# Kernel tuning notes

Hardware: AMD Instinct MI355X
Metric: run time of the kernel (lower is better)

Reference implementation:

```python
import jax, jax.numpy as jnp
import numpy as np

N_LAYERS, H, D, DH = 4, 16, 1024, 64
V_FR, V_EN = 32000, 32000
L_FR, L_EN, B = 513, 512, 2


def _pos_enc(x):
    # x: [L, B, D]; pe[i,j] = sin(i/10000^(j/D)) if j even else cos(i/10000^((j-1)/D))
    L, _, D_ = x.shape
    pos = jnp.arange(L, dtype=jnp.float32)[:, None]
    j = jnp.arange(D_)
    ang = pos / jnp.power(10000.0, (j - (j % 2)).astype(jnp.float32) / D_)
    pe = jnp.where(j % 2 == 0, jnp.sin(ang), jnp.cos(ang))
    return x + pe[:, None, :]


def _ln(x, g, b):
    mu = jnp.mean(x, -1, keepdims=True)
    var = jnp.mean((x - mu) ** 2, -1, keepdims=True)
    return (x - mu) * jax.lax.rsqrt(var + 1e-5) * g + b


def _mha(q_in, k_in, v_in, w, bias, causal):
    # w: [3, H, D, dh], bias: [3, H, dh]
    dh = w.shape[-1]
    Q = jnp.einsum('bld,hde->bhle', q_in, w[0]) + bias[0][None, :, None, :]
    K = jnp.einsum('bmd,hde->bhme', k_in, w[1]) + bias[1][None, :, None, :]
    V = jnp.einsum('bmd,hde->bhme', v_in, w[2]) + bias[2][None, :, None, :]
    s = jnp.einsum('bhle,bhme->bhlm', Q, K) / jnp.sqrt(jnp.float32(dh))
    if causal:
        m = jnp.tril(jnp.ones((s.shape[-2], s.shape[-1]), bool))
        s = jnp.where(m, s, -jnp.inf)
    a = jax.nn.softmax(s, axis=-1)
    o = jnp.einsum('bhlm,bhme->bhle', a, V)
    b_, h_, l_, dh_ = o.shape
    return o.transpose(0, 2, 1, 3).reshape(b_, l_, h_ * dh_)


def setup_inputs() -> dict:
    key = jax.random.key(0)
    ks = jax.random.split(key, 24)
    s = 0.02
    rn = lambda k, shp: jax.random.normal(k, shp, jnp.float32) * s
    return {
        'fr': jax.random.randint(ks[0], (L_FR, B), 0, V_FR),
        'en': jax.random.randint(ks[1], (L_EN, B), 0, V_EN),
        'emb_fr': rn(ks[2], (V_FR, D)),
        'emb_en': rn(ks[3], (V_EN, D)),
        'enc_qkv_w': rn(ks[4], (N_LAYERS, 3, H, D, DH)),
        'enc_qkv_b': rn(ks[5], (N_LAYERS, 3, H, DH)),
        'enc_fc1_w': rn(ks[6], (N_LAYERS, D, D)),
        'enc_fc1_b': rn(ks[7], (N_LAYERS, D)),
        'enc_fc2_w': rn(ks[8], (N_LAYERS, D, D)),
        'enc_fc2_b': rn(ks[9], (N_LAYERS, D)),
        'enc_ln_g': jnp.ones((N_LAYERS, 2, D)) + rn(ks[10], (N_LAYERS, 2, D)),
        'enc_ln_b': rn(ks[11], (N_LAYERS, 2, D)),
        'dec_self_qkv_w': rn(ks[12], (N_LAYERS, 3, H, D, DH)),
        'dec_self_qkv_b': rn(ks[13], (N_LAYERS, 3, H, DH)),
        'dec_cross_qkv_w': rn(ks[14], (N_LAYERS, 3, H, D, DH)),
        'dec_cross_qkv_b': rn(ks[15], (N_LAYERS, 3, H, DH)),
        'dec_fc1_w': rn(ks[16], (N_LAYERS, D, D)),
        'dec_fc1_b': rn(ks[17], (N_LAYERS, D)),
        'dec_fc2_w': rn(ks[18], (N_LAYERS, D, D)),
        'dec_fc2_b': rn(ks[19], (N_LAYERS, D)),
        'dec_ln_g': jnp.ones((N_LAYERS, 3, D)) + rn(ks[20], (N_LAYERS, 3, D)),
        'dec_ln_b': rn(ks[21], (N_LAYERS, 3, D)),
        'out_w': rn(ks[22], (D, V_EN)),
        'out_b': rn(ks[23], (V_EN,)),
    }


def reference(fr, en, emb_fr, emb_en, enc_qkv_w, enc_qkv_b, enc_fc1_w, enc_fc1_b,
              enc_fc2_w, enc_fc2_b, enc_ln_g, enc_ln_b, dec_self_qkv_w,
              dec_self_qkv_b, dec_cross_qkv_w, dec_cross_qkv_b, dec_fc1_w,
              dec_fc1_b, dec_fc2_w, dec_fc2_b, dec_ln_g, dec_ln_b, out_w, out_b):
    # Encoder (dropout p=0 -> identity in eval math)
    x = _pos_enc(emb_fr[fr[1:]]).transpose(1, 0, 2)  # [B, L_src, D]
    for n in range(N_LAYERS):
        a = _mha(x, x, x, enc_qkv_w[n], enc_qkv_b[n], causal=False)
        x = _ln(x + a, enc_ln_g[n, 0], enc_ln_b[n, 0])
        h = jnp.maximum(x @ enc_fc1_w[n] + enc_fc1_b[n], 0.0) @ enc_fc2_w[n] + enc_fc2_b[n]
        x = _ln(x + h, enc_ln_g[n, 1], enc_ln_b[n, 1])
    enc_out = x
    # Decoder
    y = _pos_enc(emb_en[en]).transpose(1, 0, 2)  # [B, L_tgt, D]
    for n in range(N_LAYERS):
        a = _mha(y, y, y, dec_self_qkv_w[n], dec_self_qkv_b[n], causal=True)
        y = _ln(y + a, dec_ln_g[n, 0], dec_ln_b[n, 0])
        c = _mha(y, enc_out, enc_out, dec_cross_qkv_w[n], dec_cross_qkv_b[n], causal=False)
        y = _ln(y + c, dec_ln_g[n, 1], dec_ln_b[n, 1])
        h = jnp.maximum(y @ dec_fc1_w[n] + dec_fc1_b[n], 0.0) @ dec_fc2_w[n] + dec_fc2_b[n]
        y = _ln(y + h, dec_ln_g[n, 2], dec_ln_b[n, 2])
    return y @ out_w + out_b  # [B, L_tgt, V_EN]
```

## Files before the change

kernel.cpp:

```cpp
#include <hip/hip_runtime.h>
#include <stdint.h>
#include <stddef.h>

typedef unsigned short u16;
typedef __attribute__((ext_vector_type(8))) short bf16x8;
typedef __attribute__((ext_vector_type(4))) float f32x4;

#define DEV __device__ __forceinline__

DEV float b2f(u16 u) { union { float f; uint32_t i; } v; v.i = ((uint32_t)u) << 16; return v.f; }
DEV u16 f2b(float f) {
  uint32_t x = __float_as_uint(f);
  x += 0x7fffu + ((x >> 16) & 1u);
  return (u16)(x >> 16);
}
DEV bf16x8 ld8f(const float* f) {
  float4 a = *(const float4*)f;
  float4 b = *(const float4*)(f + 4);
  bf16x8 r;
  ((u16*)&r)[0] = f2b(a.x); ((u16*)&r)[1] = f2b(a.y);
  ((u16*)&r)[2] = f2b(a.z); ((u16*)&r)[3] = f2b(a.w);
  ((u16*)&r)[4] = f2b(b.x); ((u16*)&r)[5] = f2b(b.y);
  ((u16*)&r)[6] = f2b(b.z); ((u16*)&r)[7] = f2b(b.w);
  return r;
}
DEV void gload16(const u16* g, u16* l) {
  __builtin_amdgcn_global_load_lds((const __attribute__((address_space(1))) void*)g,
                                   (__attribute__((address_space(3))) void*)l, 16, 0, 0);
}
DEV f32x4 mfma16(bf16x8 a, bf16x8 b, f32x4 c) {
  return __builtin_amdgcn_mfma_f32_16x16x32_bf16(a, b, c, 0, 0, 0);
}

__global__ __launch_bounds__(256) void transpose_w(const float* __restrict__ src,
                                                   u16* __restrict__ dst, int K, int N) {
  __shared__ u16 t[32][33];
  int tx = threadIdx.x, ty = threadIdx.y;
  int k0 = blockIdx.x * 32, n0 = blockIdx.y * 32;
  size_t base = (size_t)blockIdx.z * K * N;
#pragma unroll
  for (int i = 0; i < 4; i++) {
    int k = ty + 8 * i;
    t[k][tx] = f2b(src[base + (size_t)(k0 + k) * N + n0 + tx]);
  }
  __syncthreads();
#pragma unroll
  for (int i = 0; i < 4; i++) {
    int n = ty + 8 * i;
    dst[base + (size_t)(n0 + n) * K + k0 + tx] = t[tx][n];
  }
}

__global__ __launch_bounds__(256) void transpose_qkvT(const float* __restrict__ s0,
                                                      const float* __restrict__ s1,
                                                      const float* __restrict__ s2,
                                                      u16* __restrict__ dst) {
  int z = blockIdx.z;
  const float* src = (z < 192) ? s0 : (z < 384) ? s1 : s2;
  int zi = (z < 192) ? z : (z < 384) ? z - 192 : z - 384;
  size_t sbase = (size_t)zi * 65536;
  size_t dbase = (size_t)z * 65536;
  __shared__ u16 t[32][33];
  int tx = threadIdx.x, ty = threadIdx.y;
  int k0 = blockIdx.x * 32, n0 = blockIdx.y * 32;
#pragma unroll
  for (int i = 0; i < 4; i++) {
    int k = ty + 8 * i;
    t[k][tx] = f2b(src[sbase + (size_t)(k0 + k) * 64 + n0 + tx]);
  }
  __syncthreads();
#pragma unroll
  for (int i = 0; i < 4; i++) {
    int n = ty + 8 * i;
    dst[dbase + (size_t)(n0 + n) * 1024 + k0 + tx] = t[tx][n];
  }
}

__global__ __launch_bounds__(256) void transpose_fcT(const float* __restrict__ s0,
                                                     const float* __restrict__ s1,
                                                     const float* __restrict__ s2,
                                                     const float* __restrict__ s3,
                                                     u16* __restrict__ dst) {
  int z = blockIdx.z;
  const float* src = (z < 4) ? s0 : (z < 8) ? s1 : (z < 12) ? s2 : s3;
  size_t sbase = (size_t)(z & 3) * 1048576;
  size_t dbase = (size_t)z * 1048576;
  __shared__ u16 t[32][33];
  int tx = threadIdx.x, ty = threadIdx.y;
  int k0 = blockIdx.x * 32, n0 = blockIdx.y * 32;
#pragma unroll
  for (int i = 0; i < 4; i++) {
    int k = ty + 8 * i;
    t[k][tx] = f2b(src[sbase + (size_t)(k0 + k) * 1024 + n0 + tx]);
  }
  __syncthreads();
#pragma unroll
  for (int i = 0; i < 4; i++) {
    int n = ty + 8 * i;
    dst[dbase + (size_t)(n0 + n) * 1024 + k0 + tx] = t[tx][n];
  }
}

__global__ __launch_bounds__(256) void embed_k(const int* __restrict__ tok, const float* __restrict__ emb,
                                               float* __restrict__ o32, u16* __restrict__ ob, int shift) {
  int row = blockIdx.x;
  int b = row >> 9, l = row & 511;
  int tk = tok[(size_t)(l + shift) * 2 + b];
  const float* e = emb + (size_t)tk * 1024;
  const float c0 = -9.210340371976184f / 1024.f;
#pragma unroll
  for (int i = 0; i < 4; i++) {
    int d = threadIdx.x + i * 256;
    int j2 = d & ~1;
    float ang = (float)l * expf(c0 * (float)j2);
    float pe = (d & 1) ? cosf(ang) : sinf(ang);
    float rv = e[d] + pe;
    o32[(size_t)row * 1024 + d] = rv;
    ob[(size_t)row * 1024 + d] = f2b(rv);
  }
}

__global__ __launch_bounds__(256) void ln_k(const float* d,
                                            const float* __restrict__ g, const float* __restrict__ bb,
                                            float* o32, u16* __restrict__ ob) {
  int row = blockIdx.x;
  int tid = threadIdx.x;
  const float4 dv = ((const float4*)(d + (size_t)row * 1024))[tid];
  float v[4] = {dv.x, dv.y, dv.z, dv.w};
  float s = 0.f, s2 = 0.f;
#pragma unroll
  for (int i = 0; i < 4; i++) { s += v[i]; s2 += v[i] * v[i]; }
#pragma unroll
  for (int off = 1; off < 64; off <<= 1) {
    s += __shfl_xor(s, off);
    s2 += __shfl_xor(s2, off);
  }
  __shared__ float red[8];
  int wid = tid >> 6;
  if ((tid & 63) == 0) { red[wid * 2] = s; red[wid * 2 + 1] = s2; }
  __syncthreads();
  s = red[0] + red[2] + red[4] + red[6];
  s2 = red[1] + red[3] + red[5] + red[7];
  float mu = s * (1.f / 1024.f);
  float var = s2 * (1.f / 1024.f) - mu * mu;
  float inv = rsqrtf(var + 1e-5f);
  const float4 gv = ((const float4*)g)[tid];
  const float4 bv = ((const float4*)bb)[tid];
  float4 ov;
  ov.x = (v[0] - mu) * inv * gv.x + bv.x;
  ov.y = (v[1] - mu) * inv * gv.y + bv.y;
  ov.z = (v[2] - mu) * inv * gv.z + bv.z;
  ov.w = (v[3] - mu) * inv * gv.w + bv.w;
  ((float4*)(o32 + (size_t)row * 1024))[tid] = ov;
  uint2 p;
  p.x = (uint32_t)f2b(ov.x) | ((uint32_t)f2b(ov.y) << 16);
  p.y = (uint32_t)f2b(ov.z) | ((uint32_t)f2b(ov.w) << 16);
  ((uint2*)(ob + (size_t)row * 1024))[tid] = p;
}

template <bool RELU>
__global__ __launch_bounds__(256) void gemm_fc(const u16* __restrict__ A, const u16* __restrict__ BT,
                                               const float* __restrict__ bias,
                                               const float* __restrict__ resid, void* __restrict__ out,
                                               int N, int K) {
  __shared__ __align__(16) u16 lA[2][2][64 * 32];
  __shared__ __align__(16) u16 lB[2][2][64 * 32];
  int bx = blockIdx.x, by = blockIdx.y;
  int tid = threadIdx.x, lane = tid & 63, wid = tid >> 6;
  int l15 = lane & 15, lg = lane >> 4;
  int bm = by * 64, bn = bx * 64;
  int wr = (wid >> 1) * 32, wc = (wid & 1) * 32;
  f32x4 acc[2][2] = {};
  int r_s = tid >> 2, c_s = tid & 3;
  auto stage = [&](int pp, int kt) {
#pragma unroll
    for (int s = 0; s < 2; s++) {
      gload16(A + (size_t)(bm + r_s) * K + kt + s * 32 + c_s * 8, &lA[pp][s][(size_t)(wid * 64) * 8]);
      gload16(BT + (size_t)(bn + r_s) * K + kt + s * 32 + c_s * 8, &lB[pp][s][(size_t)(wid * 64) * 8]);
    }
  };
  int nt = K >> 6;
  stage(0, 0);
  int pp = 0;
  for (int t = 0; t < nt; t++) {
    if (t + 1 < nt) {
      stage(pp ^ 1, (t + 1) * 64);
      asm volatile("s_waitcnt vmcnt(4)" ::: "memory");
    } else {
      asm volatile("s_waitcnt vmcnt(0)" ::: "memory");
    }
    __builtin_amdgcn_s_barrier();
#pragma unroll
    for (int s = 0; s < 2; s++) {
      bf16x8 af[2], bf_[2];
#pragma unroll
      for (int m = 0; m < 2; m++) af[m] = *(const bf16x8*)&lA[pp][s][(wr + m * 16 + l15) * 32 + lg * 8];
#pragma unroll
      for (int n = 0; n < 2; n++) bf_[n] = *(const bf16x8*)&lB[pp][s][(wc + n * 16 + l15) * 32 + lg * 8];
#pragma unroll
      for (int m = 0; m < 2; m++)
#pragma unroll
        for (int n = 0; n < 2; n++) acc[m][n] = mfma16(af[m], bf_[n], acc[m][n]);
    }
    __builtin_amdgcn_s_barrier();
    pp ^= 1;
  }
#pragma unroll
  for (int n = 0; n < 2; n++) {
    int col = bn + wc + n * 16 + l15;
    float bv = bias[col];
#pragma unroll
    for (int m = 0; m < 2; m++) {
#pragma unroll
      for (int r = 0; r < 4; r++) {
        int row = bm + wr + m * 16 + lg * 4 + r;
        float v = acc[m][n][r] + bv;
        if (RELU) ((u16*)out)[(size_t)row * N + col] = f2b(fmaxf(v, 0.f));
        else ((float*)out)[(size_t)row * N + col] = v + resid[(size_t)row * N + col];
      }
    }
  }
}

__global__ __launch_bounds__(256) void gemm_qkv3(const u16* __restrict__ Aq, const u16* __restrict__ Akv,
                                                 const u16* __restrict__ WT, const float* __restrict__ bias,
                                                 u16* __restrict__ Qo, u16* __restrict__ Ko,
                                                 u16* __restrict__ Vto) {
  __shared__ __align__(16) u16 lA[2][2][64 * 32];
  __shared__ __align__(16) u16 lB[2][2][64 * 32];
  int bx = blockIdx.x, by = blockIdx.y;
  int t_ = bx >> 4;
  const u16* A = (t_ == 0) ? Aq : Akv;
  int tid = threadIdx.x, lane = tid & 63, wid = tid >> 6;
  int l15 = lane & 15, lg = lane >> 4;
  int bm = by * 64, bn = bx * 64;
  int wr = (wid >> 1) * 32, wc = (wid & 1) * 32;
  f32x4 acc[2][2] = {};
  int r_s = tid >> 2, c_s = tid & 3;
  auto stage = [&](int pp, int kt) {
#pragma unroll
    for (int s = 0; s < 2; s++) {
      gload16(A + (size_t)(bm + r_s) * 1024 + kt + s * 32 + c_s * 8, &lA[pp][s][(size_t)(wid * 64) * 8]);
      gload16(WT + (size_t)(bn + r_s) * 1024 + kt + s * 32 + c_s * 8, &lB[pp][s][(size_t)(wid * 64) * 8]);
    }
  };
  stage(0, 0);
  int pp = 0;
  for (int t = 0; t < 16; t++) {
    if (t + 1 < 16) {
      stage(pp ^ 1, (t + 1) * 64);
      asm volatile("s_waitcnt vmcnt(4)" ::: "memory");
    } else {
      asm volatile("s_waitcnt vmcnt(0)" ::: "memory");
    }
    __builtin_amdgcn_s_barrier();
#pragma unroll
    for (int s = 0; s < 2; s++) {
      bf16x8 af[2], bf_[2];
#pragma unroll
      for (int m = 0; m < 2; m++) af[m] = *(const bf16x8*)&lA[pp][s][(wr + m * 16 + l15) * 32 + lg * 8];
#pragma unroll
      for (int n = 0; n < 2; n++) bf_[n] = *(const bf16x8*)&lB[pp][s][(wc + n * 16 + l15) * 32 + lg * 8];
#pragma unroll
      for (int m = 0; m < 2; m++)
#pragma unroll
        for (int n = 0; n < 2; n++) acc[m][n] = mfma16(af[m], bf_[n], acc[m][n]);
    }
    __builtin_amdgcn_s_barrier();
    pp ^= 1;
  }
#pragma unroll
  for (int n = 0; n < 2; n++) {
    int col = bn + wc + n * 16 + l15;
    int h = (col >> 6) & 15, e = col & 63;
    float bv = bias[col];
#pragma unroll
    for (int m = 0; m < 2; m++) {
#pragma unroll
      for (int r = 0; r < 4; r++) {
        int row = bm + wr + m * 16 + lg * 4 + r;
        int b = row >> 9, l = row & 511;
        u16 vbv = f2b(acc[m][n][r] + bv);
        size_t bhead = (size_t)b * 16 + h;
        if (t_ == 0) Qo[(bhead * 512 + l) * 64 + e] = vbv;
        else if (t_ == 1) Ko[(bhead * 512 + l) * 64 + e] = vbv;
        else Vto[(bhead * 64 + e) * 512 + l] = vbv;
      }
    }
  }
}

template <int BM, int BN, int RS, int RM>
__global__ __launch_bounds__(256) void gemm_p3(const u16* __restrict__ A, const u16* __restrict__ BT,
                                               const float* __restrict__ bias, float* __restrict__ out,
                                               int N, int K) {
  constexpr int FM = BM / 32, FN = BN / 32;
  constexpr int L = BM / 64 + BN / 64;
  __shared__ __align__(16) u16 lA[3][BM * 32];
  __shared__ __align__(16) u16 lB[3][BN * 32];
  int b = blockIdx.x;
  int p = (b & 7) + 8 * (b >> RS);
  if (p >= N / BN) return;
  int bx = p, by = (b >> 3) & RM;
  int tid = threadIdx.x, lane = tid & 63, wid = tid >> 6;
  int l15 = lane & 15, lg = lane >> 4;
  int bm = by * BM, bn = bx * BN;
  int wr = (wid >> 1) * (BM / 2), wc = (wid & 1) * (BN / 2);
  f32x4 acc[FM][FN] = {};
  int r_s = tid >> 2, c_s = tid & 3;
  auto stage = [&](int buf, int kt) {
#pragma unroll
    for (int i = 0; i < BM / 64; i++)
      gload16(A + (size_t)(bm + i * 64 + r_s) * K + kt + c_s * 8, &lA[buf][(i * 256 + wid * 64) * 8]);
#pragma unroll
    for (int i = 0; i < BN / 64; i++)
      gload16(BT + (size_t)(bn + i * 64 + r_s) * K + kt + c_s * 8, &lB[buf][(i * 256 + wid * 64) * 8]);
  };
  int nt = K >> 5;
  stage(0, 0);
  stage(1, 32);
  asm volatile("s_waitcnt vmcnt(%0)" ::"n"(L) : "memory");
  __builtin_amdgcn_s_barrier();
  int cur = 0;
  for (int t = 0; t < nt; t++) {
    if (t + 2 < nt) stage(cur == 0 ? 2 : cur - 1, (t + 2) * 32);
    bf16x8 af[FM], bf_[FN];
#pragma unroll
    for (int m = 0; m < FM; m++) af[m] = *(const bf16x8*)&lA[cur][(wr + m * 16 + l15) * 32 + lg * 8];
#pragma unroll
    for (int n = 0; n < FN; n++) bf_[n] = *(const bf16x8*)&lB[cur][(wc + n * 16 + l15) * 32 + lg * 8];
#pragma unroll
    for (int m = 0; m < FM; m++)
#pragma unroll
      for (int n = 0; n < FN; n++) acc[m][n] = mfma16(af[m], bf_[n], acc[m][n]);
    if (t + 2 < nt) {
      asm volatile("s_waitcnt vmcnt(%0)" ::"n"(L) : "memory");
    } else if (t + 1 < nt) {
      asm volatile("s_waitcnt vmcnt(0)" ::: "memory");
    }
    if (t + 1 < nt) __builtin_amdgcn_s_barrier();
    cur = (cur == 2) ? 0 : cur + 1;
  }
#pragma unroll
  for (int n = 0; n < FN; n++) {
    int col = bn + wc + n * 16 + l15;
    float bv = bias[col];
#pragma unroll
    for (int m = 0; m < FM; m++) {
#pragma unroll
      for (int r = 0; r < 4; r++) {
        int row = bm + wr + m * 16 + lg * 4 + r;
        out[(size_t)row * N + col] = acc[m][n][r] + bv;
      }
    }
  }
}

__global__ __launch_bounds__(256) void gemm_bn(const u16* __restrict__ A, const float* __restrict__ B,
                                               const float* __restrict__ bias, float* __restrict__ out,
                                               int N, int K) {
  __shared__ __align__(16) u16 lA[128 * 32];
  __shared__ __align__(16) u16 lBn[32 * 128];
  int b = blockIdx.x;
  int p = (b & 7) + 8 * (b >> 6);
  if (p >= N / 128) return;
  int by = (b >> 3) & 7;
  int tid = threadIdx.x, lane = tid & 63;
  int wid = tid >> 6;
  int l15 = lane & 15, lg = lane >> 4;
  int bm = by * 128, bn = p * 128;
  int wr = (wid >> 1) * 64, wc = (wid & 1) * 64;
  f32x4 acc[4][4] = {};
  int r_s = tid >> 2, c_s = tid & 3;
  int br = tid >> 4, bc = tid & 15;
  for (int kt = 0; kt < K; kt += 32) {
    bf16x8 va[2], vb[2];
#pragma unroll
    for (int it = 0; it < 2; it++) {
      va[it] = *(const bf16x8*)&A[(size_t)(bm + it * 64 + r_s) * K + kt + c_s * 8];
      vb[it] = ld8f(B + (size_t)(kt + it * 16 + br) * N + bn + bc * 8);
    }
    __syncthreads();
#pragma unroll
    for (int it = 0; it < 2; it++) {
      *(bf16x8*)&lA[(size_t)(it * 256 + tid) * 8] = va[it];
      *(bf16x8*)&lBn[(size_t)(it * 256 + tid) * 8] = vb[it];
    }
    __syncthreads();
    bf16x8 af[4], bfr[4];
#pragma unroll
    for (int m = 0; m < 4; m++) af[m] = *(const bf16x8*)&lA[(wr + m * 16 + l15) * 32 + lg * 8];
#pragma unroll
    for (int n = 0; n < 4; n++) {
#pragma unroll
      for (int j = 0; j < 8; j++)
        ((short*)&bfr[n])[j] = (short)lBn[(lg * 8 + j) * 128 + wc + n * 16 + l15];
    }
#pragma unroll
    for (int m = 0; m < 4; m++)
#pragma unroll
      for (int n = 0; n < 4; n++) acc[m][n] = mfma16(af[m], bfr[n], acc[m][n]);
  }
#pragma unroll
  for (int n = 0; n < 4; n++) {
    int col = bn + wc + n * 16 + l15;
    float bv = bias[col];
#pragma unroll
    for (int m = 0; m < 4; m++) {
#pragma unroll
      for (int r = 0; r < 4; r++) {
        int row = bm + wr + m * 16 + lg * 4 + r;
        out[(size_t)row * N + col] = acc[m][n][r] + bv;
      }
    }
  }
}

template <bool CAUSAL>
__global__ __launch_bounds__(256) void attn_k(const u16* __restrict__ Qb, const u16* __restrict__ Kb,
                                              const u16* __restrict__ Vtb, const float* __restrict__ R,
                                              float* __restrict__ Ob) {
  int bh = blockIdx.y;
  int tid = threadIdx.x, lane = tid & 63, w = tid >> 6;
  int l15 = lane & 15, lg = lane >> 4;
  int q0 = blockIdx.x * 64 + w * 16;
  const u16* Qh = Qb + (size_t)bh * 512 * 64;
  const u16* Kh = Kb + (size_t)bh * 512 * 64;
  const u16* Vh = Vtb + (size_t)bh * 64 * 512;
  __shared__ __align__(16) u16 P[4][16 * 40];
  u16* Pw = &P[w][0];
  bf16x8 qa0 = *(const bf16x8*)&Qh[(size_t)(q0 + l15) * 64 + lg * 8];
  bf16x8 qa1 = *(const bf16x8*)&Qh[(size_t)(q0 + l15) * 64 + 32 + lg * 8];
  f32x4 acc[4];
#pragma unroll
  for (int c = 0; c < 4; c++) acc[c] = (f32x4){0.f, 0.f, 0.f, 0.f};
  float ls[4] = {0.f, 0.f, 0.f, 0.f};
  int ktend = CAUSAL ? ((q0 + 15) >> 5) : 15;
  bf16x8 kn00 = *(const bf16x8*)&Kh[(size_t)(l15) * 64 + lg * 8];
  bf16x8 kn01 = *(const bf16x8*)&Kh[(size_t)(l15) * 64 + 32 + lg * 8];
  bf16x8 kn10 = *(const bf16x8*)&Kh[(size_t)(16 + l15) * 64 + lg * 8];
  bf16x8 kn11 = *(const bf16x8*)&Kh[(size_t)(16 + l15) * 64 + 32 + lg * 8];
  for (int kt = 0; kt <= ktend; kt++) {
    int kv = kt * 32;
    bf16x8 c00 = kn00, c01 = kn01, c10 = kn10, c11 = kn11;
    if (kt < ktend) {
      int kv2 = kv + 32;
      kn00 = *(const bf16x8*)&Kh[(size_t)(kv2 + l15) * 64 + lg * 8];
      kn01 = *(const bf16x8*)&Kh[(size_t)(kv2 + l15) * 64 + 32 + lg * 8];
      kn10 = *(const bf16x8*)&Kh[(size_t)(kv2 + 16 + l15) * 64 + lg * 8];
      kn11 = *(const bf16x8*)&Kh[(size_t)(kv2 + 16 + l15) * 64 + 32 + lg * 8];
    }
    f32x4 z = (f32x4){0.f, 0.f, 0.f, 0.f};
    f32x4 s0 = mfma16(qa0, c00, z);
    s0 = mfma16(qa1, c01, s0);
    f32x4 s1 = mfma16(qa0, c10, z);
    s1 = mfma16(qa1, c11, s1);
#pragma unroll
    for (int r = 0; r < 4; r++) {
      float a0 = s0[r] * 0.125f, a1 = s1[r] * 0.125f;
      if (CAUSAL) {
        int rowg = q0 + lg * 4 + r;
        if (kv + l15 > rowg) a0 = -1e30f;
        if (kv + 16 + l15 > rowg) a1 = -1e30f;
      }
      float p0 = __expf(a0), p1 = __expf(a1);
      ls[r] += p0 + p1;
      int prow = lg * 4 + r;
      Pw[prow * 40 + l15] = f2b(p0);
      Pw[prow * 40 + 16 + l15] = f2b(p1);
    }
    bf16x8 pa = *(const bf16x8*)&Pw[l15 * 40 + lg * 8];
#pragma unroll
    for (int c = 0; c < 4; c++) {
      bf16x8 vb = *(const bf16x8*)&Vh[(size_t)(c * 16 + l15) * 512 + kv + lg * 8];
      acc[c] = mfma16(pa, vb, acc[c]);
    }
  }
#pragma unroll
  for (int r = 0; r < 4; r++) {
#pragma unroll
    for (int off = 1; off < 16; off <<= 1) ls[r] += __shfl_xor(ls[r], off);
  }
  int b = bh >> 4, h = bh & 15;
#pragma unroll
  for (int r = 0; r < 4; r++) {
    float inv = 1.f / ls[r];
    int rowg = q0 + lg * 4 + r;
    size_t off0 = (size_t)(b * 512 + rowg) * 1024 + h * 64;
#pragma unroll
    for (int c = 0; c < 4; c++)
      Ob[off0 + c * 16 + l15] = R[off0 + c * 16 + l15] + acc[c][r] * inv;
  }
}

extern "C" void kernel_launch(void* const* d_in, const int* in_sizes, int n_in,
                              void* d_out, int out_size, void* d_ws, size_t ws_size,
                              hipStream_t stream) {
  const int* fr = (const int*)d_in[0];
  const int* en = (const int*)d_in[1];
  const float* emb_fr = (const float*)d_in[2];
  const float* emb_en = (const float*)d_in[3];
  const float* enc_qkv_w = (const float*)d_in[4];
  const float* enc_qkv_b = (const float*)d_in[5];
  const float* enc_fc1_w = (const float*)d_in[6];
  const float* enc_fc1_b = (const float*)d_in[7];
  const float* enc_fc2_w = (const float*)d_in[8];
  const float* enc_fc2_b = (const float*)d_in[9];
  const float* enc_ln_g = (const float*)d_in[10];
  const float* enc_ln_bb = (const float*)d_in[11];
  const float* dec_self_qkv_w = (const float*)d_in[12];
  const float* dec_self_qkv_b = (const float*)d_in[13];
  const float* dec_cross_qkv_w = (const float*)d_in[14];
  const float* dec_cross_qkv_b = (const float*)d_in[15];
  const float* dec_fc1_w = (const float*)d_in[16];
  const float* dec_fc1_b = (const float*)d_in[17];
  const float* dec_fc2_w = (const float*)d_in[18];
  const float* dec_fc2_b = (const float*)d_in[19];
  const float* dec_ln_g = (const float*)d_in[20];
  const float* dec_ln_bb = (const float*)d_in[21];
  const float* out_w = (const float*)d_in[22];
  const float* out_b = (const float*)d_in[23];

  char* o8 = (char*)d_out;
  u16* qkvT_d = (u16*)o8;
  u16* fcT_d = (u16*)(o8 + 6291456);
  float* x32 = (float*)(o8 + 8388608);
  float* y32 = (float*)(o8 + 12582912);
  float* d32 = (float*)(o8 + 16777216);
  u16* xb = (u16*)(o8 + 20971520);
  u16* hb = (u16*)(o8 + 23068672);
  u16* Qb = (u16*)(o8 + 25165824);
  u16* Kb = (u16*)(o8 + 27262976);
  u16* Vtb = (u16*)(o8 + 29360128);

  char* w8 = (char*)d_ws;
  u16* yb = (u16*)w8;
  u16* outwT = (u16*)(w8 + 2097152);
  u16* eqkvT = (u16*)(w8 + 67633152);
  u16* dsqkvT = (u16*)(w8 + 92798976);
  u16* dcqkvT = (u16*)(w8 + 117964800);
  u16* efc1T = (u16*)(w8 + 143130624);
  u16* efc2T = (u16*)(w8 + 151519232);
  u16* dfc1T = (u16*)(w8 + 159907840);
  u16* dfc2T = (u16*)(w8 + 168296448);
  int tier = (ws_size >= 176685056u) ? 2 : (ws_size >= 67633152u) ? 1 : 0;

  dim3 tb(32, 8);
  if (tier >= 1)
    transpose_w<<<dim3(32, 1000, 1), tb, 0, stream>>>(out_w, outwT, 1024, 32000);
  if (tier == 2) {
    transpose_qkvT<<<dim3(32, 2, 576), tb, 0, stream>>>(enc_qkv_w, dec_self_qkv_w, dec_cross_qkv_w, eqkvT);
    transpose_fcT<<<dim3(32, 32, 16), tb, 0, stream>>>(enc_fc1_w, enc_fc2_w, dec_fc1_w, dec_fc2_w, efc1T);
  }

  embed_k<<<1024, 256, 0, stream>>>(fr, emb_fr, x32, xb, 1);
  embed_k<<<1024, 256, 0, stream>>>(en, emb_en, y32, yb, 0);

  for (int n = 0; n < 4; n++) {
    const u16* wqkv;
    if (tier == 2) wqkv = eqkvT + (size_t)n * 3145728;
    else {
      transpose_w<<<dim3(32, 2, 48), tb, 0, stream>>>(enc_qkv_w + (size_t)n * 48 * 65536, qkvT_d, 1024, 64);
      wqkv = qkvT_d;
    }
    gemm_qkv3<<<dim3(48, 16), 256, 0, stream>>>(xb, xb, wqkv, enc_qkv_b + (size_t)n * 3072, Qb, Kb, Vtb);
    attn_k<false><<<dim3(8, 32), 256, 0, stream>>>(Qb, Kb, Vtb, x32, d32);
    ln_k<<<1024, 256, 0, stream>>>(d32, enc_ln_g + (size_t)(n * 2) * 1024,
                                   enc_ln_bb + (size_t)(n * 2) * 1024, x32, xb);
    const u16* w1;
    if (tier == 2) w1 = efc1T + (size_t)n * 1048576;
    else {
      transpose_w<<<dim3(32, 32, 1), tb, 0, stream>>>(enc_fc1_w + (size_t)n * 1048576, fcT_d, 1024, 1024);
      w1 = fcT_d;
    }
    gemm_fc<true><<<dim3(16, 16), 256, 0, stream>>>(xb, w1, enc_fc1_b + (size_t)n * 1024,
                                                    nullptr, hb, 1024, 1024);
    const u16* w2;
    if (tier == 2) w2 = efc2T + (size_t)n * 1048576;
    else {
      transpose_w<<<dim3(32, 32, 1), tb, 0, stream>>>(enc_fc2_w + (size_t)n * 1048576, fcT_d, 1024, 1024);
      w2 = fcT_d;
    }
    gemm_fc<false><<<dim3(16, 16), 256, 0, stream>>>(hb, w2, enc_fc2_b + (size_t)n * 1024,
                                                     x32, d32, 1024, 1024);
    ln_k<<<1024, 256, 0, stream>>>(d32, enc_ln_g + (size_t)(n * 2 + 1) * 1024,
                                   enc_ln_bb + (size_t)(n * 2 + 1) * 1024, x32, xb);
  }
  for (int n = 0; n < 4; n++) {
    const u16* wq;
    if (tier == 2) wq = dsqkvT + (size_t)n * 3145728;
    else {
      transpose_w<<<dim3(32, 2, 48), tb, 0, stream>>>(dec_self_qkv_w + (size_t)n * 48 * 65536, qkvT_d, 1024, 64);
      wq = qkvT_d;
    }
    gemm_qkv3<<<dim3(48, 16), 256, 0, stream>>>(yb, yb, wq, dec_self_qkv_b + (size_t)n * 3072, Qb, Kb, Vtb);
    attn_k<true><<<dim3(8, 32), 256, 0, stream>>>(Qb, Kb, Vtb, y32, d32);
    ln_k<<<1024, 256, 0, stream>>>(d32, dec_ln_g + (size_t)(n * 3) * 1024,
                                   dec_ln_bb + (size_t)(n * 3) * 1024, y32, yb);
    if (tier == 2) wq = dcqkvT + (size_t)n * 3145728;
    else {
      transpose_w<<<dim3(32, 2, 48), tb, 0, stream>>>(dec_cross_qkv_w + (size_t)n * 48 * 65536, qkvT_d, 1024, 64);
      wq = qkvT_d;
    }
    gemm_qkv3<<<dim3(48, 16), 256, 0, stream>>>(yb, xb, wq, dec_cross_qkv_b + (size_t)n * 3072, Qb, Kb, Vtb);
    attn_k<false><<<dim3(8, 32), 256, 0, stream>>>(Qb, Kb, Vtb, y32, d32);
    ln_k<<<1024, 256, 0, stream>>>(d32, dec_ln_g + (size_t)(n * 3 + 1) * 1024,
                                   dec_ln_bb + (size_t)(n * 3 + 1) * 1024, y32, yb);
    const u16* w1;
    if (tier == 2) w1 = dfc1T + (size_t)n * 1048576;
    else {
      transpose_w<<<dim3(32, 32, 1), tb, 0, stream>>>(dec_fc1_w + (size_t)n * 1048576, fcT_d, 1024, 1024);
      w1 = fcT_d;
    }
    gemm_fc<true><<<dim3(16, 16), 256, 0, stream>>>(yb, w1, dec_fc1_b + (size_t)n * 1024,
                                                    nullptr, hb, 1024, 1024);
    const u16* w2;
    if (tier == 2) w2 = dfc2T + (size_t)n * 1048576;
    else {
      transpose_w<<<dim3(32, 32, 1), tb, 0, stream>>>(dec_fc2_w + (size_t)n * 1048576, fcT_d, 1024, 1024);
      w2 = fcT_d;
    }
    gemm_fc<false><<<dim3(16, 16), 256, 0, stream>>>(hb, w2, dec_fc2_b + (size_t)n * 1024,
                                                     y32, d32, 1024, 1024);
    ln_k<<<1024, 256, 0, stream>>>(d32, dec_ln_g + (size_t)(n * 3 + 2) * 1024,
                                   dec_ln_bb + (size_t)(n * 3 + 2) * 1024, y32, yb);
  }
  if (tier >= 1)
    gemm_p3<128, 128, 6, 7><<<dim3(2048), 256, 0, stream>>>(yb, outwT, out_b, (float*)d_out, 32000, 1024);
  else
    gemm_bn<<<dim3(2048), 256, 0, stream>>>(yb, out_w, out_b, (float*)d_out, 32000, 1024);
}
```

Baseline: 956.0 us.

## Replace output projection GEMM with 256x256 tile, 512-thread double-buffered kernel

The vocabulary projection GEMM now uses 256x256 block tiles with 8 waves per block, each wave computing a 128x64 subtile, instead of 128x128 tiles with 4 waves. Larger tiles raise arithmetic intensity and halve global loads per FLOP for the largest GEMM. In exchange the pipeline drops from triple to double buffering with two barriers per k-step, and fewer, larger blocks may reduce latency hiding and load balance across CUs.

```diff
diff --git a/kernel.cpp b/kernel.cpp
--- a/kernel.cpp
+++ b/kernel.cpp
@@ -290,66 +290,60 @@
   }
 }
 
-template <int BM, int BN, int RS, int RM>
-__global__ __launch_bounds__(256) void gemm_p3(const u16* __restrict__ A, const u16* __restrict__ BT,
-                                               const float* __restrict__ bias, float* __restrict__ out,
-                                               int N, int K) {
-  constexpr int FM = BM / 32, FN = BN / 32;
-  constexpr int L = BM / 64 + BN / 64;
-  __shared__ __align__(16) u16 lA[3][BM * 32];
-  __shared__ __align__(16) u16 lB[3][BN * 32];
+__global__ __launch_bounds__(512) void gemm_f256(const u16* __restrict__ A, const u16* __restrict__ BT,
+                                                 const float* __restrict__ bias, float* __restrict__ out,
+                                                 int N, int K) {
+  __shared__ __align__(16) u16 lA[2][256 * 32];
+  __shared__ __align__(16) u16 lB[2][256 * 32];
   int b = blockIdx.x;
-  int p = (b & 7) + 8 * (b >> RS);
-  if (p >= N / BN) return;
-  int bx = p, by = (b >> 3) & RM;
+  int p = (b & 7) + 8 * (b >> 5);
+  if (p >= N / 256) return;
+  int brow = (b >> 3) & 3;
   int tid = threadIdx.x, lane = tid & 63, wid = tid >> 6;
   int l15 = lane & 15, lg = lane >> 4;
-  int bm = by * BM, bn = bx * BN;
-  int wr = (wid >> 1) * (BM / 2), wc = (wid & 1) * (BN / 2);
-  f32x4 acc[FM][FN] = {};
+  int bm = brow * 256, bn = p * 256;
+  int wrow = (wid >> 2) * 128, wcol = (wid & 3) * 64;
+  f32x4 acc[8][4] = {};
   int r_s = tid >> 2, c_s = tid & 3;
-  auto stage = [&](int buf, int kt) {
-#pragma unroll
-    for (int i = 0; i < BM / 64; i++)
-      gload16(A + (size_t)(bm + i * 64 + r_s) * K + kt + c_s * 8, &lA[buf][(i * 256 + wid * 64) * 8]);
-#pragma unroll
-    for (int i = 0; i < BN / 64; i++)
-      gload16(BT + (size_t)(bn + i * 64 + r_s) * K + kt + c_s * 8, &lB[buf][(i * 256 + wid * 64) * 8]);
+  auto stage = [&](int pp, int kt) {
+#pragma unroll
+    for (int i = 0; i < 2; i++) {
+      gload16(A + (size_t)(bm + i * 128 + r_s) * K + kt + c_s * 8, &lA[pp][(size_t)(i * 512 + tid) * 8]);
+      gload16(BT + (size_t)(bn + i * 128 + r_s) * K + kt + c_s * 8, &lB[pp][(size_t)(i * 512 + tid) * 8]);
+    }
   };
   int nt = K >> 5;
   stage(0, 0);
-  stage(1, 32);
-  asm volatile("s_waitcnt vmcnt(%0)" ::"n"(L) : "memory");
-  __builtin_amdgcn_s_barrier();
-  int cur = 0;
+  int pp = 0;
   for (int t = 0; t < nt; t++) {
-    if (t + 2 < nt) stage(cur == 0 ? 2 : cur - 1, (t + 2) * 32);
-    bf16x8 af[FM], bf_[FN];
-#pragma unroll
-    for (int m = 0; m < FM; m++) af[m] = *(const bf16x8*)&lA[cur][(wr + m * 16 + l15) * 32 + lg * 8];
-#pragma unroll
-    for (int n = 0; n < FN; n++) bf_[n] = *(const bf16x8*)&lB[cur][(wc + n * 16 + l15) * 32 + lg * 8];
-#pragma unroll
-    for (int m = 0; m < FM; m++)
-#pragma unroll
-      for (int n = 0; n < FN; n++) acc[m][n] = mfma16(af[m], bf_[n], acc[m][n]);
-    if (t + 2 < nt) {
-      asm volatile("s_waitcnt vmcnt(%0)" ::"n"(L) : "memory");
-    } else if (t + 1 < nt) {
+    if (t + 1 < nt) {
+      stage(pp ^ 1, (t + 1) * 32);
+      asm volatile("s_waitcnt vmcnt(4)" ::: "memory");
+    } else {
       asm volatile("s_waitcnt vmcnt(0)" ::: "memory");
     }
-    if (t + 1 < nt) __builtin_amdgcn_s_barrier();
-    cur = (cur == 2) ? 0 : cur + 1;
-  }
-#pragma unroll
-  for (int n = 0; n < FN; n++) {
-    int col = bn + wc + n * 16 + l15;
+    __builtin_amdgcn_s_barrier();
+    bf16x8 af[8], bf_[4];
+#pragma unroll
+    for (int m = 0; m < 8; m++) af[m] = *(const bf16x8*)&lA[pp][(wrow + m * 16 + l15) * 32 + lg * 8];
+#pragma unroll
+    for (int n = 0; n < 4; n++) bf_[n] = *(const bf16x8*)&lB[pp][(wcol + n * 16 + l15) * 32 + lg * 8];
+#pragma unroll
+    for (int m = 0; m < 8; m++)
+#pragma unroll
+      for (int n = 0; n < 4; n++) acc[m][n] = mfma16(af[m], bf_[n], acc[m][n]);
+    __builtin_amdgcn_s_barrier();
+    pp ^= 1;
+  }
+#pragma unroll
+  for (int n = 0; n < 4; n++) {
+    int col = bn + wcol + n * 16 + l15;
     float bv = bias[col];
 #pragma unroll
-    for (int m = 0; m < FM; m++) {
+    for (int m = 0; m < 8; m++) {
 #pragma unroll
       for (int r = 0; r < 4; r++) {
-        int row = bm + wr + m * 16 + lg * 4 + r;
+        int row = bm + wrow + m * 16 + lg * 4 + r;
         out[(size_t)row * N + col] = acc[m][n][r] + bv;
       }
     }
@@ -626,7 +620,7 @@
                                    dec_ln_bb + (size_t)(n * 3 + 2) * 1024, y32, yb);
   }
   if (tier >= 1)
-    gemm_p3<128, 128, 6, 7><<<dim3(2048), 256, 0, stream>>>(yb, outwT, out_b, (float*)d_out, 32000, 1024);
+    gemm_f256<<<dim3(512), 512, 0, stream>>>(yb, outwT, out_b, (float*)d_out, 32000, 1024);
   else
     gemm_bn<<<dim3(2048), 256, 0, stream>>>(yb, out_w, out_b, (float*)d_out, 32000, 1024);
 }
```

Result: no change. 962.3 us (+0.7%).
